# Optimization experiments

Measured on AMD Instinct MI355X. Metric: run time of the kernel, lower is better.

The kernel has to match this reference:

```python
import jax, jax.numpy as jnp
import numpy as np

IN_F = 4096
OUT_F = 4096
TOKENS = 8192
NNZ_PER_ROW = 64
NNZ = OUT_F * NNZ_PER_ROW
ALPHA = 1.0  # kill-switch default (full intelligence)


def setup_inputs() -> dict:
    key = jax.random.key(0)
    k1, k2, k3, k4, k5 = jax.random.split(key, 5)
    x = jax.random.normal(k1, (TOKENS, IN_F), dtype=jnp.float32)
    # nibble-packed int4 weights: each uint8 holds two int4 values (low|high<<4)
    base_weight = jax.random.randint(k2, (OUT_F, IN_F // 2), 0, 256, dtype=jnp.int32)
    # per-output-row dequant scales (fp16 in the module; fp32 math here)
    base_scales = jax.random.uniform(k3, (OUT_F,), dtype=jnp.float32) * 0.01 + 1e-4
    ortho_values = jax.random.normal(k4, (NNZ,), dtype=jnp.float32) * 0.02
    ortho_col_indices = jax.random.randint(k5, (NNZ,), 0, IN_F, dtype=jnp.int32)
    # CSR row pointer: exactly NNZ_PER_ROW nonzeros per output row
    ortho_row_ptr = (jnp.arange(OUT_F + 1, dtype=jnp.int32) * NNZ_PER_ROW)
    return {
        'x': x,
        'base_weight': base_weight,
        'base_scales': base_scales,
        'ortho_values': ortho_values,
        'ortho_col_indices': ortho_col_indices,
        'ortho_row_ptr': ortho_row_ptr,
    }


def _dequant_int4(base_weight, base_scales, in_f):
    # unpack nibbles: even flat index = low nibble, odd = high nibble (row-major)
    out_f = base_weight.shape[0]
    low = base_weight & 15
    high = (base_weight >> 4) & 15
    w = jnp.stack([low, high], axis=-1).reshape(out_f, in_f)  # [out, in] in 0..15
    w = jnp.where(w >= 8, w - 16, w)  # signed int4 in [-8, 7]
    return w.astype(base_scales.dtype) * base_scales[:, None]  # [out, in]


def _densify_csr(values, col_indices, row_ptr, out_f, in_f):
    nnz = values.shape[0]
    row_ids = jnp.searchsorted(row_ptr, jnp.arange(nnz, dtype=jnp.int32), side='right') - 1
    return jnp.zeros((out_f, in_f), values.dtype).at[row_ids, col_indices].add(values)


def reference(x, base_weight, base_scales, ortho_values, ortho_col_indices, ortho_row_ptr):
    out_f = base_weight.shape[0]
    in_f = x.shape[-1]
    W_base = _dequant_int4(base_weight, base_scales, in_f)          # [out, in]
    W_ortho = _densify_csr(ortho_values, ortho_col_indices, ortho_row_ptr, out_f, in_f)
    # Y = X @ W_base^T + alpha * X @ W_ortho^T  (fused as a single GEMM)
    W = W_base + ALPHA * W_ortho
    return x @ W.T  # [tokens, out]
```

## Files before the change

### kernel.cpp

```cpp
#include <hip/hip_runtime.h>
#include <hip/hip_bf16.h>

#define TOKENS 8192
#define IN_F   4096
#define OUT_F  4096

#define BM 256
#define BN 256
#define KSTEP 128
#define NT (IN_F / KSTEP)

typedef int   i32x4  __attribute__((ext_vector_type(4)));

#define BARRIER() asm volatile("s_barrier" ::: "memory")
#define VMCNT4()  asm volatile("s_waitcnt vmcnt(4)" ::: "memory")
#define VMCNT0()  asm volatile("s_waitcnt vmcnt(0)" ::: "memory")

__device__ __forceinline__ void gload_lds16(const void* g, void* l) {
  __builtin_amdgcn_global_load_lds(
      (const __attribute__((address_space(1))) void*)g,
      (__attribute__((address_space(3))) void*)l, 16, 0, 0);
}

__device__ __forceinline__ float blockmax256(float m, float* red) {
#pragma unroll
  for (int off = 32; off; off >>= 1)
    m = fmaxf(m, __shfl_xor(m, off, 64));
  if ((threadIdx.x & 63) == 0) red[threadIdx.x >> 6] = m;
  __syncthreads();
  return fmaxf(fmaxf(red[0], red[1]), fmaxf(red[2], red[3]));
}

__device__ __forceinline__ int pack4(const float* v, float inv) {
  unsigned w = 0;
#pragma unroll
  for (int b = 0; b < 4; ++b) {
    int q = __float2int_rn(fmaxf(fminf(v[b] * inv, 127.f), -127.f));
    w |= ((unsigned)(unsigned char)(signed char)q) << (8 * b);
  }
  return (int)w;
}

__global__ __launch_bounds__(256) void prep_w_i8(
    const int* __restrict__ bw, const float* __restrict__ scales,
    const float* __restrict__ vals, const int* __restrict__ cols,
    const int* __restrict__ rptr, signed char* __restrict__ Wq,
    float* __restrict__ sw) {
  __shared__ float row[IN_F];
  __shared__ float red[4];
  const int n = blockIdx.x;
  const int tid = threadIdx.x;
  const float s = scales[n];
  const int* bwr = bw + (size_t)n * (IN_F / 2);
#pragma unroll
  for (int it = 0; it < (IN_F / 2) / 256; ++it) {
    int j = it * 256 + tid;
    int p = bwr[j];
    int lo = p & 15;        lo = (lo >= 8) ? lo - 16 : lo;
    int hi = (p >> 4) & 15; hi = (hi >= 8) ? hi - 16 : hi;
    row[2 * j]     = (float)lo * s;
    row[2 * j + 1] = (float)hi * s;
  }
  __syncthreads();
  const int b = rptr[n], e = rptr[n + 1];
  for (int t = b + tid; t < e; t += 256)
    atomicAdd(&row[cols[t]], vals[t]);
  __syncthreads();
  float m = 0.f;
#pragma unroll
  for (int it = 0; it < IN_F / 256; ++it)
    m = fmaxf(m, fabsf(row[it * 256 + tid]));
  const float mm  = fmaxf(blockmax256(m, red), 1e-30f);
  const float inv = 127.f / mm;
  int4 w;
  w.x = pack4(&row[tid * 16 + 0],  inv);
  w.y = pack4(&row[tid * 16 + 4],  inv);
  w.z = pack4(&row[tid * 16 + 8],  inv);
  w.w = pack4(&row[tid * 16 + 12], inv);
  *(int4*)(Wq + (size_t)n * IN_F + tid * 16) = w;
  if (tid == 0) sw[n] = mm / 127.f;
}

__global__ __launch_bounds__(256) void cvt_x_i8(
    const float4* __restrict__ x, int* __restrict__ xq,
    float* __restrict__ sx) {
  __shared__ float red[4];
  const int tok = blockIdx.x;
  const int tid = threadIdx.x;
  const float4* xr = x + (size_t)tok * (IN_F / 4);
  float4 v[4];
  float m = 0.f;
#pragma unroll
  for (int j = 0; j < 4; ++j) {
    v[j] = xr[j * 256 + tid];
    m = fmaxf(m, fmaxf(fmaxf(fabsf(v[j].x), fabsf(v[j].y)),
                       fmaxf(fabsf(v[j].z), fabsf(v[j].w))));
  }
  const float mm  = fmaxf(blockmax256(m, red), 1e-30f);
  const float inv = 127.f / mm;
  int* xo = xq + (size_t)tok * (IN_F / 4);
#pragma unroll
  for (int j = 0; j < 4; ++j) {
    float vv[4] = {v[j].x, v[j].y, v[j].z, v[j].w};
    xo[j * 256 + tid] = pack4(vv, inv);
  }
  if (tid == 0) sx[tok] = mm / 127.f;
}

__global__ __launch_bounds__(512, 2) void gemm_i8(
    const unsigned char* __restrict__ A,
    const unsigned char* __restrict__ B,
    const float* __restrict__ sx,
    const float* __restrict__ sw,
    float* __restrict__ C) {
  __shared__ __align__(16) char lds[131072];

  const int nbn = OUT_F / BN;
  const int cpx = ((TOKENS / BM) * nbn) >> 3;
  const int bid = blockIdx.x;
  const int swz = (bid & 7) * cpx + (bid >> 3);
  const int tm = swz / nbn, tn = swz % nbn;
  const long m0 = (long)tm * BM;
  const long n0 = (long)tn * BN;

  const int tid  = threadIdx.x;
  const int lane = tid & 63;
  const int wid  = tid >> 6;
  const int wr   = wid >> 2;
  const int wc   = wid & 3;

  const int p0 = tid * 16;
  const int p1 = p0 + 8192;
  const int lin0 = p0 ^ (((p0 >> 9) & 1) << 5);
  const int lin1 = p1 ^ (((p1 >> 9) & 1) << 5);
  const int r0  = (((p0 >> 10) & 15) << 4) | ((lin0 >> 6) & 15);
  const int r1  = (((p1 >> 10) & 15) << 4) | ((lin1 >> 6) & 15);
  const int kb0 = lin0 & 63;
  const int kb1 = lin1 & 63;

  const unsigned char* Abase = A + m0 * IN_F;
  const unsigned char* Bbase = B + n0 * IN_F;

  int laneoff = ((lane & 15) << 6) | ((lane >> 4) << 4);
  laneoff ^= ((laneoff >> 9) & 1) << 5;

#define STAGE_A(nb, kt, h)                                                     \
  do {                                                                         \
    gload_lds16(Abase + (size_t)r0 * IN_F + (kt) * 128 + (h) * 64 + kb0,       \
                lds + (nb) * 65536 + (h) * 16384 + p0);                        \
    gload_lds16(Abase + (size_t)r1 * IN_F + (kt) * 128 + (h) * 64 + kb1,       \
                lds + (nb) * 65536 + (h) * 16384 + p1);                        \
  } while (0)
#define STAGE_B(nb, kt, h)                                                     \
  do {                                                                         \
    gload_lds16(Bbase + (size_t)r0 * IN_F + (kt) * 128 + (h) * 64 + kb0,       \
                lds + (nb) * 65536 + 32768 + (h) * 16384 + p0);                \
    gload_lds16(Bbase + (size_t)r1 * IN_F + (kt) * 128 + (h) * 64 + kb1,       \
                lds + (nb) * 65536 + 32768 + (h) * 16384 + p1);                \
  } while (0)

  i32x4 acc[8][4];
#pragma unroll
  for (int i = 0; i < 8; ++i)
#pragma unroll
    for (int j = 0; j < 4; ++j) acc[i][j] = (i32x4)0;

  i32x4 av1[8], av2[8], bv1[4], bv2[4];

  STAGE_A(0, 0, 0);
  STAGE_B(0, 0, 0);
  STAGE_A(0, 0, 1);
  STAGE_B(0, 0, 1);
  VMCNT4();
  BARRIER();
#pragma unroll
  for (int i = 0; i < 8; ++i)
    av1[i] = *(const i32x4*)(lds + (wr * 8 + i) * 1024 + laneoff);
#pragma unroll
  for (int j = 0; j < 4; ++j)
    bv1[j] = *(const i32x4*)(lds + 32768 + (wc * 4 + j) * 1024 + laneoff);

  for (int t = 0; t < NT; ++t) {
    const int b  = t & 1;
    const int nb = b ^ 1;
    const char* bufA  = lds + b * 65536;
    const char* bufB  = bufA + 32768;
    const char* nbufA = lds + nb * 65536;
    const char* nbufB = nbufA + 32768;
    const bool pf = (t + 1 < NT);

    VMCNT0();
    BARRIER();
    __builtin_amdgcn_s_setprio(1);
    if (pf) { STAGE_A(nb, t + 1, 0); STAGE_B(nb, t + 1, 0); }
#pragma unroll
    for (int i = 0; i < 8; ++i)
      av2[i] = *(const i32x4*)(bufA + 16384 + (wr * 8 + i) * 1024 + laneoff);
#pragma unroll
    for (int j = 0; j < 4; ++j)
      bv2[j] = *(const i32x4*)(bufB + 16384 + (wc * 4 + j) * 1024 + laneoff);
#pragma unroll
    for (int i = 0; i < 8; ++i)
#pragma unroll
      for (int j = 0; j < 4; ++j)
        acc[i][j] = __builtin_amdgcn_mfma_i32_16x16x64_i8(av1[i], bv1[j], acc[i][j], 0, 0, 0);
    __builtin_amdgcn_s_setprio(0);

    VMCNT0();
    BARRIER();
    __builtin_amdgcn_s_setprio(1);
    if (pf) {
      STAGE_A(nb, t + 1, 1);
      STAGE_B(nb, t + 1, 1);
#pragma unroll
      for (int i = 0; i < 8; ++i)
        av1[i] = *(const i32x4*)(nbufA + (wr * 8 + i) * 1024 + laneoff);
#pragma unroll
      for (int j = 0; j < 4; ++j)
        bv1[j] = *(const i32x4*)(nbufB + (wc * 4 + j) * 1024 + laneoff);
    }
#pragma unroll
    for (int i = 0; i < 8; ++i)
#pragma unroll
      for (int j = 0; j < 4; ++j)
        acc[i][j] = __builtin_amdgcn_mfma_i32_16x16x64_i8(av2[i], bv2[j], acc[i][j], 0, 0, 0);
    __builtin_amdgcn_s_setprio(0);
  }
#undef STAGE_A
#undef STAGE_B

  const int er = (lane >> 4) * 4;
  const int ec = lane & 15;
#pragma unroll
  for (int i = 0; i < 8; ++i) {
    long rbase = m0 + wr * 128 + i * 16 + er;
    float sxq[4];
#pragma unroll
    for (int q = 0; q < 4; ++q) sxq[q] = sx[rbase + q];
#pragma unroll
    for (int j = 0; j < 4; ++j) {
      long cbase = n0 + wc * 64 + j * 16 + ec;
      const float swc = sw[cbase];
#pragma unroll
      for (int q = 0; q < 4; ++q)
        C[(rbase + q) * OUT_F + cbase] = (float)acc[i][j][q] * sxq[q] * swc;
    }
  }
}

__global__ __launch_bounds__(256) void fallback_kernel(
    const float* __restrict__ x, const int* __restrict__ bw,
    const float* __restrict__ scales, const float* __restrict__ vals,
    const int* __restrict__ cols, const int* __restrict__ rptr,
    float* __restrict__ out) {
  const int oc  = blockIdx.x * 64 + (threadIdx.x & 63);
  const int tok = blockIdx.y * 4 + (threadIdx.x >> 6);
  const float s = scales[oc];
  const int* bwr = bw + (size_t)oc * (IN_F / 2);
  const float* xr = x + (size_t)tok * IN_F;
  float acc = 0.f;
  for (int j = 0; j < IN_F / 2; ++j) {
    int p = bwr[j];
    int lo = p & 15;        lo = (lo >= 8) ? lo - 16 : lo;
    int hi = (p >> 4) & 15; hi = (hi >= 8) ? hi - 16 : hi;
    acc += ((float)lo * s) * xr[2 * j] + ((float)hi * s) * xr[2 * j + 1];
  }
  const int b = rptr[oc], e = rptr[oc + 1];
  for (int t = b; t < e; ++t) acc += vals[t] * xr[cols[t]];
  out[(size_t)tok * OUT_F + oc] = acc;
}

extern "C" void kernel_launch(void* const* d_in, const int* in_sizes, int n_in,
                              void* d_out, int out_size, void* d_ws, size_t ws_size,
                              hipStream_t stream) {
  const float* x      = (const float*)d_in[0];
  const int*   bw     = (const int*)d_in[1];
  const float* scales = (const float*)d_in[2];
  const float* vals   = (const float*)d_in[3];
  const int*   cols   = (const int*)d_in[4];
  const int*   rptr   = (const int*)d_in[5];
  float* out = (float*)d_out;

  const size_t wq_off = 0;
  const size_t xq_off = (size_t)OUT_F * IN_F;
  const size_t sw_off = xq_off + (size_t)TOKENS * IN_F;
  const size_t sx_off = sw_off + 65536;
  const size_t need   = sx_off + 65536;

  if (ws_size >= need) {
    signed char* Wq = (signed char*)d_ws + wq_off;
    signed char* Xq = (signed char*)d_ws + xq_off;
    float* sw = (float*)((char*)d_ws + sw_off);
    float* sx = (float*)((char*)d_ws + sx_off);
    prep_w_i8<<<OUT_F, 256, 0, stream>>>(bw, scales, vals, cols, rptr, Wq, sw);
    cvt_x_i8<<<TOKENS, 256, 0, stream>>>((const float4*)x, (int*)Xq, sx);
    gemm_i8<<<(TOKENS / BM) * (OUT_F / BN), 512, 0, stream>>>(
        (const unsigned char*)Xq, (const unsigned char*)Wq, sx, sw, out);
  } else {
    dim3 grid(OUT_F / 64, TOKENS / 4);
    fallback_kernel<<<grid, 256, 0, stream>>>(x, bw, scales, vals, cols, rptr, out);
  }
}
```

Before: 191.9 us.

## Shrink GEMM tile to 256x128 with triple-buffered BK=64 LDS pipeline

Replaces the 256x256 double-buffered, two-half K-step int8 GEMM with a 256x128 tile using BK=64 and a three-buffer rotating LDS ring. Loads run two stages ahead, and a partial vmcnt wait lets the next stage's loads stay in flight. LDS use drops from 128KB to 72KB and the launch bound rises to 4 blocks per CU, so more blocks can be resident to hide latency. The cost is lower arithmetic intensity per tile, more global traffic for A, and one barrier per smaller K-step.

```diff
diff --git a/kernel.cpp b/kernel.cpp
--- a/kernel.cpp
+++ b/kernel.cpp
@@ -6,14 +6,16 @@
 #define OUT_F  4096
 
 #define BM 256
-#define BN 256
-#define KSTEP 128
-#define NT (IN_F / KSTEP)
+#define BN 128
+#define BK 64
+#define NT (IN_F / BK)
+#define BUFSZ 24576
+#define BOFF  16384
 
 typedef int   i32x4  __attribute__((ext_vector_type(4)));
 
 #define BARRIER() asm volatile("s_barrier" ::: "memory")
-#define VMCNT4()  asm volatile("s_waitcnt vmcnt(4)" ::: "memory")
+#define VMCNT3()  asm volatile("s_waitcnt vmcnt(3)" ::: "memory")
 #define VMCNT0()  asm volatile("s_waitcnt vmcnt(0)" ::: "memory")
 
 __device__ __forceinline__ void gload_lds16(const void* g, void* l) {
@@ -107,13 +109,13 @@
   if (tid == 0) sx[tok] = mm / 127.f;
 }
 
-__global__ __launch_bounds__(512, 2) void gemm_i8(
+__global__ __launch_bounds__(512, 4) void gemm_i8(
     const unsigned char* __restrict__ A,
     const unsigned char* __restrict__ B,
     const float* __restrict__ sx,
     const float* __restrict__ sw,
     float* __restrict__ C) {
-  __shared__ __align__(16) char lds[131072];
+  __shared__ __align__(16) char lds[3 * BUFSZ];
 
   const int nbn = OUT_F / BN;
   const int cpx = ((TOKENS / BM) * nbn) >> 3;
@@ -126,8 +128,8 @@
   const int tid  = threadIdx.x;
   const int lane = tid & 63;
   const int wid  = tid >> 6;
-  const int wr   = wid >> 2;
-  const int wc   = wid & 3;
+  const int wr   = wid >> 1;
+  const int wc   = wid & 1;
 
   const int p0 = tid * 16;
   const int p1 = p0 + 8192;
@@ -138,102 +140,68 @@
   const int kb0 = lin0 & 63;
   const int kb1 = lin1 & 63;
 
+  const int rA0 = r0;
+  const int rA1 = (((p1 >> 10) & 15) << 4) | ((lin1 >> 6) & 15);
+  const long offA0 = (long)rA0 * IN_F + kb0;
+  const long offA1 = (long)rA1 * IN_F + kb1;
+  const long offB0 = (long)r0  * IN_F + kb0;
+
   const unsigned char* Abase = A + m0 * IN_F;
   const unsigned char* Bbase = B + n0 * IN_F;
 
   int laneoff = ((lane & 15) << 6) | ((lane >> 4) << 4);
   laneoff ^= ((laneoff >> 9) & 1) << 5;
 
-#define STAGE_A(nb, kt, h)                                                     \
-  do {                                                                         \
-    gload_lds16(Abase + (size_t)r0 * IN_F + (kt) * 128 + (h) * 64 + kb0,       \
-                lds + (nb) * 65536 + (h) * 16384 + p0);                        \
-    gload_lds16(Abase + (size_t)r1 * IN_F + (kt) * 128 + (h) * 64 + kb1,       \
-                lds + (nb) * 65536 + (h) * 16384 + p1);                        \
+#define STAGE(dst, kt)                                          \
+  do {                                                          \
+    gload_lds16(Abase + offA0 + (kt) * 64, (dst) + p0);         \
+    gload_lds16(Abase + offA1 + (kt) * 64, (dst) + p1);         \
+    gload_lds16(Bbase + offB0 + (kt) * 64, (dst) + BOFF + p0);  \
   } while (0)
-#define STAGE_B(nb, kt, h)                                                     \
-  do {                                                                         \
-    gload_lds16(Bbase + (size_t)r0 * IN_F + (kt) * 128 + (h) * 64 + kb0,       \
-                lds + (nb) * 65536 + 32768 + (h) * 16384 + p0);                \
-    gload_lds16(Bbase + (size_t)r1 * IN_F + (kt) * 128 + (h) * 64 + kb1,       \
-                lds + (nb) * 65536 + 32768 + (h) * 16384 + p1);                \
-  } while (0)
-
-  i32x4 acc[8][4];
-#pragma unroll
-  for (int i = 0; i < 8; ++i)
+
+  i32x4 acc[4][4];
+#pragma unroll
+  for (int i = 0; i < 4; ++i)
 #pragma unroll
     for (int j = 0; j < 4; ++j) acc[i][j] = (i32x4)0;
 
-  i32x4 av1[8], av2[8], bv1[4], bv2[4];
-
-  STAGE_A(0, 0, 0);
-  STAGE_B(0, 0, 0);
-  STAGE_A(0, 0, 1);
-  STAGE_B(0, 0, 1);
-  VMCNT4();
-  BARRIER();
-#pragma unroll
-  for (int i = 0; i < 8; ++i)
-    av1[i] = *(const i32x4*)(lds + (wr * 8 + i) * 1024 + laneoff);
-#pragma unroll
-  for (int j = 0; j < 4; ++j)
-    bv1[j] = *(const i32x4*)(lds + 32768 + (wc * 4 + j) * 1024 + laneoff);
+  char* bR = lds;
+  char* bM = lds + BUFSZ;
+  char* bS = lds + 2 * BUFSZ;
+
+  STAGE(bR, 0);
+  STAGE(bM, 1);
 
   for (int t = 0; t < NT; ++t) {
-    const int b  = t & 1;
-    const int nb = b ^ 1;
-    const char* bufA  = lds + b * 65536;
-    const char* bufB  = bufA + 32768;
-    const char* nbufA = lds + nb * 65536;
-    const char* nbufB = nbufA + 32768;
-    const bool pf = (t + 1 < NT);
-
-    VMCNT0();
+    if (t < NT - 1) { VMCNT3(); } else { VMCNT0(); }
     BARRIER();
+    if (t + 2 < NT) STAGE(bS, t + 2);
+
+    i32x4 av[4], bv[4];
+#pragma unroll
+    for (int i = 0; i < 4; ++i)
+      av[i] = *(const i32x4*)(bR + (wr * 4 + i) * 1024 + laneoff);
+#pragma unroll
+    for (int j = 0; j < 4; ++j)
+      bv[j] = *(const i32x4*)(bR + BOFF + (wc * 4 + j) * 1024 + laneoff);
+
     __builtin_amdgcn_s_setprio(1);
-    if (pf) { STAGE_A(nb, t + 1, 0); STAGE_B(nb, t + 1, 0); }
-#pragma unroll
-    for (int i = 0; i < 8; ++i)
-      av2[i] = *(const i32x4*)(bufA + 16384 + (wr * 8 + i) * 1024 + laneoff);
-#pragma unroll
-    for (int j = 0; j < 4; ++j)
-      bv2[j] = *(const i32x4*)(bufB + 16384 + (wc * 4 + j) * 1024 + laneoff);
-#pragma unroll
-    for (int i = 0; i < 8; ++i)
+#pragma unroll
+    for (int i = 0; i < 4; ++i)
 #pragma unroll
       for (int j = 0; j < 4; ++j)
-        acc[i][j] = __builtin_amdgcn_mfma_i32_16x16x64_i8(av1[i], bv1[j], acc[i][j], 0, 0, 0);
+        acc[i][j] = __builtin_amdgcn_mfma_i32_16x16x64_i8(av[i], bv[j], acc[i][j], 0, 0, 0);
     __builtin_amdgcn_s_setprio(0);
 
-    VMCNT0();
-    BARRIER();
-    __builtin_amdgcn_s_setprio(1);
-    if (pf) {
-      STAGE_A(nb, t + 1, 1);
-      STAGE_B(nb, t + 1, 1);
-#pragma unroll
-      for (int i = 0; i < 8; ++i)
-        av1[i] = *(const i32x4*)(nbufA + (wr * 8 + i) * 1024 + laneoff);
-#pragma unroll
-      for (int j = 0; j < 4; ++j)
-        bv1[j] = *(const i32x4*)(nbufB + (wc * 4 + j) * 1024 + laneoff);
-    }
-#pragma unroll
-    for (int i = 0; i < 8; ++i)
-#pragma unroll
-      for (int j = 0; j < 4; ++j)
-        acc[i][j] = __builtin_amdgcn_mfma_i32_16x16x64_i8(av2[i], bv2[j], acc[i][j], 0, 0, 0);
-    __builtin_amdgcn_s_setprio(0);
-  }
-#undef STAGE_A
-#undef STAGE_B
+    char* tmp = bR; bR = bM; bM = bS; bS = tmp;
+  }
+#undef STAGE
 
   const int er = (lane >> 4) * 4;
   const int ec = lane & 15;
 #pragma unroll
-  for (int i = 0; i < 8; ++i) {
-    long rbase = m0 + wr * 128 + i * 16 + er;
+  for (int i = 0; i < 4; ++i) {
+    long rbase = m0 + wr * 64 + i * 16 + er;
     float sxq[4];
 #pragma unroll
     for (int q = 0; q < 4; ++q) sxq[q] = sx[rbase + q];
```

After: 202.9 us. 1.06x slower.

## Switch int8 GEMM to 32x32x32 MFMA with four-phase pipelined LDS schedule

Applied to the files above, without the earlier changes.

The int8 GEMM main loop moves from 16x16x64 MFMA tiles to 32x32x32 MFMA tiles, so each wave now holds a 4x2 grid of 16-register accumulators. The LDS read offsets and the epilogue's row/column mapping are reworked to match the 32x32 operand and output layout. Each k-tile is split into four sub-steps, alternating register buffers and interleaving the global->LDS stages for A and B halves, with partial vmcnt(2) waits instead of full drains. The aim is fewer LDS reads per MFMA and better overlap of loads with compute, at the cost of more barriers and a more fragile wait/barrier ordering.

```diff
diff --git a/kernel.cpp b/kernel.cpp
--- a/kernel.cpp
+++ b/kernel.cpp
@@ -10,11 +10,15 @@
 #define KSTEP 128
 #define NT (IN_F / KSTEP)
 
-typedef int   i32x4  __attribute__((ext_vector_type(4)));
+typedef int   i32x4   __attribute__((ext_vector_type(4)));
+typedef int   i32x16  __attribute__((ext_vector_type(16)));
 
 #define BARRIER() asm volatile("s_barrier" ::: "memory")
 #define VMCNT4()  asm volatile("s_waitcnt vmcnt(4)" ::: "memory")
+#define VMCNT2()  asm volatile("s_waitcnt vmcnt(2)" ::: "memory")
 #define VMCNT0()  asm volatile("s_waitcnt vmcnt(0)" ::: "memory")
+
+#define MFMA32(a, b, c) __builtin_amdgcn_mfma_i32_32x32x32_i8((a), (b), (c), 0, 0, 0)
 
 __device__ __forceinline__ void gload_lds16(const void* g, void* l) {
   __builtin_amdgcn_global_load_lds(
@@ -141,8 +145,10 @@
   const unsigned char* Abase = A + m0 * IN_F;
   const unsigned char* Bbase = B + n0 * IN_F;
 
-  int laneoff = ((lane & 15) << 6) | ((lane >> 4) << 4);
-  laneoff ^= ((laneoff >> 9) & 1) << 5;
+  const int lo = ((lane >> 4) & 1) * 1024 + (lane & 15) * 64 + (lane >> 5) * 16;
+  const int xr_ = ((lo >> 9) & 1) << 5;
+  const char* rd0 = lds + (lo ^ xr_);
+  const char* rd1 = lds + ((lo + 32) ^ xr_);
 
 #define STAGE_A(nb, kt, h)                                                     \
   do {                                                                         \
@@ -159,13 +165,36 @@
                 lds + (nb) * 65536 + 32768 + (h) * 16384 + p1);                \
   } while (0)
 
-  i32x4 acc[8][4];
-#pragma unroll
-  for (int i = 0; i < 8; ++i)
-#pragma unroll
-    for (int j = 0; j < 4; ++j) acc[i][j] = (i32x4)0;
-
-  i32x4 av1[8], av2[8], bv1[4], bv2[4];
+#define LD_A(dst, base, boff, s)                                               \
+  do {                                                                         \
+    _Pragma("unroll")                                                          \
+    for (int f = 0; f < 4; ++f)                                                \
+      dst[f] = *(const i32x4*)((base) + (boff) + ((s) >> 1) * 16384 +          \
+                               (wr * 8 + f * 2) * 1024);                       \
+  } while (0)
+#define LD_B(dst, base, boff, s)                                               \
+  do {                                                                         \
+    _Pragma("unroll")                                                          \
+    for (int g = 0; g < 2; ++g)                                                \
+      dst[g] = *(const i32x4*)((base) + (boff) + 32768 + ((s) >> 1) * 16384 +  \
+                               (wc * 4 + g * 2) * 1024);                       \
+  } while (0)
+#define MFMA_CLUSTER(av, bv)                                                   \
+  do {                                                                         \
+    _Pragma("unroll")                                                          \
+    for (int f = 0; f < 4; ++f)                                                \
+      _Pragma("unroll")                                                        \
+      for (int g = 0; g < 2; ++g)                                              \
+        acc[f][g] = MFMA32(av[f], bv[g], acc[f][g]);                           \
+  } while (0)
+
+  i32x16 acc[4][2];
+#pragma unroll
+  for (int f = 0; f < 4; ++f)
+#pragma unroll
+    for (int g = 0; g < 2; ++g) acc[f][g] = (i32x16)0;
+
+  i32x4 av1[4], av2[4], av3[4], av4[4], bv1[2], bv2[2], bv3[2], bv4[2];
 
   STAGE_A(0, 0, 0);
   STAGE_B(0, 0, 0);
@@ -173,77 +202,76 @@
   STAGE_B(0, 0, 1);
   VMCNT4();
   BARRIER();
-#pragma unroll
-  for (int i = 0; i < 8; ++i)
-    av1[i] = *(const i32x4*)(lds + (wr * 8 + i) * 1024 + laneoff);
-#pragma unroll
-  for (int j = 0; j < 4; ++j)
-    bv1[j] = *(const i32x4*)(lds + 32768 + (wc * 4 + j) * 1024 + laneoff);
+  LD_A(av1, rd0, 0, 0);
+  LD_B(bv1, rd0, 0, 0);
 
   for (int t = 0; t < NT; ++t) {
     const int b  = t & 1;
     const int nb = b ^ 1;
-    const char* bufA  = lds + b * 65536;
-    const char* bufB  = bufA + 32768;
-    const char* nbufA = lds + nb * 65536;
-    const char* nbufB = nbufA + 32768;
+    const int boff  = b * 65536;
+    const int nboff = nb * 65536;
     const bool pf = (t + 1 < NT);
 
-    VMCNT0();
     BARRIER();
     __builtin_amdgcn_s_setprio(1);
-    if (pf) { STAGE_A(nb, t + 1, 0); STAGE_B(nb, t + 1, 0); }
-#pragma unroll
-    for (int i = 0; i < 8; ++i)
-      av2[i] = *(const i32x4*)(bufA + 16384 + (wr * 8 + i) * 1024 + laneoff);
-#pragma unroll
-    for (int j = 0; j < 4; ++j)
-      bv2[j] = *(const i32x4*)(bufB + 16384 + (wc * 4 + j) * 1024 + laneoff);
-#pragma unroll
-    for (int i = 0; i < 8; ++i)
-#pragma unroll
-      for (int j = 0; j < 4; ++j)
-        acc[i][j] = __builtin_amdgcn_mfma_i32_16x16x64_i8(av1[i], bv1[j], acc[i][j], 0, 0, 0);
+    if (pf) STAGE_A(nb, t + 1, 0);
+    LD_A(av2, rd1, boff, 1);
+    LD_B(bv2, rd1, boff, 1);
+    MFMA_CLUSTER(av1, bv1);
     __builtin_amdgcn_s_setprio(0);
 
-    VMCNT0();
+    if (pf) { VMCNT2(); } else { VMCNT0(); }
+    BARRIER();
+    __builtin_amdgcn_s_setprio(1);
+    if (pf) STAGE_B(nb, t + 1, 0);
+    LD_A(av3, rd0, boff, 2);
+    LD_B(bv3, rd0, boff, 2);
+    MFMA_CLUSTER(av2, bv2);
+    __builtin_amdgcn_s_setprio(0);
+
+    BARRIER();
+    __builtin_amdgcn_s_setprio(1);
+    if (pf) STAGE_A(nb, t + 1, 1);
+    LD_A(av4, rd1, boff, 3);
+    LD_B(bv4, rd1, boff, 3);
+    MFMA_CLUSTER(av3, bv3);
+    __builtin_amdgcn_s_setprio(0);
+
+    if (pf) { VMCNT2(); } else { VMCNT0(); }
     BARRIER();
     __builtin_amdgcn_s_setprio(1);
     if (pf) {
-      STAGE_A(nb, t + 1, 1);
       STAGE_B(nb, t + 1, 1);
-#pragma unroll
-      for (int i = 0; i < 8; ++i)
-        av1[i] = *(const i32x4*)(nbufA + (wr * 8 + i) * 1024 + laneoff);
-#pragma unroll
-      for (int j = 0; j < 4; ++j)
-        bv1[j] = *(const i32x4*)(nbufB + (wc * 4 + j) * 1024 + laneoff);
+      LD_A(av1, rd0, nboff, 0);
+      LD_B(bv1, rd0, nboff, 0);
     }
-#pragma unroll
-    for (int i = 0; i < 8; ++i)
-#pragma unroll
-      for (int j = 0; j < 4; ++j)
-        acc[i][j] = __builtin_amdgcn_mfma_i32_16x16x64_i8(av2[i], bv2[j], acc[i][j], 0, 0, 0);
+    MFMA_CLUSTER(av4, bv4);
     __builtin_amdgcn_s_setprio(0);
   }
 #undef STAGE_A
 #undef STAGE_B
-
-  const int er = (lane >> 4) * 4;
-  const int ec = lane & 15;
-#pragma unroll
-  for (int i = 0; i < 8; ++i) {
-    long rbase = m0 + wr * 128 + i * 16 + er;
-    float sxq[4];
-#pragma unroll
-    for (int q = 0; q < 4; ++q) sxq[q] = sx[rbase + q];
-#pragma unroll
-    for (int j = 0; j < 4; ++j) {
-      long cbase = n0 + wc * 64 + j * 16 + ec;
-      const float swc = sw[cbase];
-#pragma unroll
-      for (int q = 0; q < 4; ++q)
-        C[(rbase + q) * OUT_F + cbase] = (float)acc[i][j][q] * sxq[q] * swc;
+#undef LD_A
+#undef LD_B
+#undef MFMA_CLUSTER
+
+  const int ec = lane & 31;
+  const int rq = (lane >> 5) * 4;
+#pragma unroll
+  for (int f = 0; f < 4; ++f) {
+    const long rb = m0 + wr * 128 + f * 32;
+    float sxv[16];
+#pragma unroll
+    for (int r = 0; r < 16; ++r)
+      sxv[r] = sx[rb + (r & 3) + 8 * (r >> 2) + rq];
+#pragma unroll
+    for (int g = 0; g < 2; ++g) {
+      const long cb = n0 + wc * 64 + g * 32 + ec;
+      const float swc = sw[cb];
+#pragma unroll
+      for (int r = 0; r < 16; ++r) {
+        const long row = rb + (r & 3) + 8 * (r >> 2) + rq;
+        C[row * OUT_F + cb] = (float)acc[f][g][r] * sxv[r] * swc;
+      }
     }
   }
 }
```

Result: slower. 196.0 us (+2.2%).
